# Kernel optimization log

Measured on AMD Instinct MI355X. Metric: run time of the kernel, lower is better.

Reference implementation:

```python
import jax, jax.numpy as jnp
import numpy as np
from jax import lax

S = 8  # num_segments


def conv2d(x, w, stride=1, pad=0):
    return lax.conv_general_dilated(x, w, (stride, stride), [(pad, pad), (pad, pad)],
                                    dimension_numbers=('NCHW', 'OIHW', 'NCHW'))


def bn(x, g, b):  # inference-mode BatchNorm as per-channel affine
    return x * g[None, :, None, None] + b[None, :, None, None]


def conv1x1(x, w):  # w: [O, C]
    return jnp.einsum('bchw,oc->bohw', x, w)


def avgpool3s2(x):  # AvgPool2d(3, stride=2, padding=1), count_include_pad=True
    s = lax.reduce_window(x, 0.0, lax.add, (1, 1, 3, 3), (1, 1, 2, 2),
                          [(0, 0), (0, 0), (1, 1), (1, 1)])
    return s / 9.0


def navigation_mask(x, gumbel, nav_w, nav_bn_g, nav_bn_b, gs_w, gs_b, temp=1.0):
    B = x.shape[0]
    y = x.mean(axis=(2, 3))                                    # global avg pool -> [B, C]
    g = jnp.maximum(y @ nav_w.T * nav_bn_g + nav_bn_b, 0.0)    # conv_pool (1x1) + BN + ReLU -> [B, 2]
    g = g.reshape(B // S, S, 2)
    # grouped 1x1 conv (groups=S) == per-segment 2x2 matmul; gs_w: [S, out, in]
    logits = jnp.einsum('bsi,sji->bsj', g, gs_w) + gs_b        # [nvid, S, 2]
    y_soft = jax.nn.softmax((logits + gumbel) / temp, axis=-1)
    hard = jax.nn.one_hot(jnp.argmax(y_soft, axis=-1), 2, dtype=y_soft.dtype)
    y_st = hard + y_soft - lax.stop_gradient(y_soft)           # straight-through hard gumbel
    return y_st[:, :, 1].reshape(B, 1, 1, 1)                   # channel 1 = focal-on


def setup_inputs() -> dict:
    key = jax.random.key(0)
    ks = iter(jax.random.split(key, 48))

    def rn(shape, scale=0.05):
        return jax.random.normal(next(ks), shape, dtype=jnp.float32) * scale

    B, C_in, C_out, C_amp, H = 128, 64, 128, 64, 56
    u = jax.random.uniform(next(ks), (B // S, S, 2), minval=1e-6, maxval=1.0 - 1e-6)
    return dict(
        x=rn((B, C_in, H, H), 1.0),
        gumbel=(-jnp.log(-jnp.log(u))).astype(jnp.float32),
        nav_w=rn((2, C_in)), nav_bn_g=jnp.ones((2,), jnp.float32), nav_bn_b=jnp.zeros((2,), jnp.float32),
        gs_w=rn((S, 2, 2)),
        gs_b=jnp.tile(jnp.array([1.0, 10.0], dtype=jnp.float32), (S, 1)),  # bias init from source
        ba_w1=rn((C_amp, C_in, 3, 3)), ba_g1=jnp.ones((C_amp,), jnp.float32), ba_b1=jnp.zeros((C_amp,), jnp.float32),
        ba_w2=rn((C_amp, C_amp, 3, 3)), ba_g2=jnp.ones((C_amp,), jnp.float32), ba_b2=jnp.zeros((C_amp,), jnp.float32),
        bf_wd=rn((C_out, C_in)), bf_gd=jnp.ones((C_out,), jnp.float32), bf_bd=jnp.zeros((C_out,), jnp.float32),
        bf_w1=rn((C_out, C_in, 3, 3)), bf_g1=jnp.ones((C_out,), jnp.float32), bf_b1=jnp.zeros((C_out,), jnp.float32),
        bf_w2=rn((C_out, C_out, 3, 3)), bf_g2=jnp.ones((C_out,), jnp.float32), bf_b2=jnp.zeros((C_out,), jnp.float32),
        bt_w=rn((C_out, C_amp)), bt_g=jnp.ones((C_out,), jnp.float32), bt_b=jnp.zeros((C_out,), jnp.float32),
        att_w1=rn((C_out // 16, C_out), 0.01), att_w2=rn((C_out, C_out // 16), 0.01),
        fu_w1=rn((C_out, C_out, 3, 3)), fu_g1=jnp.ones((C_out,), jnp.float32), fu_b1=jnp.zeros((C_out,), jnp.float32),
        fu_w2=rn((C_out, C_out, 3, 3)), fu_g2=jnp.ones((C_out,), jnp.float32), fu_b2=jnp.zeros((C_out,), jnp.float32),
    )


def reference(x, gumbel, nav_w, nav_bn_g, nav_bn_b, gs_w, gs_b,
              ba_w1, ba_g1, ba_b1, ba_w2, ba_g2, ba_b2,
              bf_wd, bf_gd, bf_bd, bf_w1, bf_g1, bf_b1, bf_w2, bf_g2, bf_b2,
              bt_w, bt_g, bt_b, att_w1, att_w2,
              fu_w1, fu_g1, fu_b1, fu_w2, fu_g2, fu_b2):
    mask = navigation_mask(x, gumbel, nav_w, nav_bn_g, nav_bn_b, gs_w, gs_b)
    # ample branch: stride-2 low-res residual block (last_relu=False)
    res_l = avgpool3s2(x)
    h = jnp.maximum(bn(conv2d(x, ba_w1, 2, 1), ba_g1, ba_b1), 0.0)
    x_little = bn(conv2d(h, ba_w2, 1, 1), ba_g2, ba_b2) + res_l              # [B,64,28,28]
    # focal branch: full-res residual block, branch gated per-segment by mask
    res_b = bn(conv1x1(x, bf_wd), bf_gd, bf_bd)
    h = jnp.maximum(bn(conv2d(x, bf_w1, 1, 1), bf_g1, bf_b1), 0.0)
    x_big = res_b + mask * bn(conv2d(h, bf_w2, 1, 1), bf_g2, bf_b2)          # [B,128,56,56]
    x_little = bn(conv1x1(x_little, bt_w), bt_g, bt_b)
    x_little = jnp.repeat(jnp.repeat(x_little, 2, axis=2), 2, axis=3)        # F.interpolate nearest
    # SE-style dynamic fusion
    y = (x_little + x_big).mean(axis=(2, 3))                                 # [B,128]
    att = jax.nn.sigmoid(jnp.maximum(y @ att_w1.T, 0.0) @ att_w2.T)[:, :, None, None]
    out = jnp.maximum(att * x_little + (1.0 - att) * x_big, 0.0)
    # fusion block: residual, last_relu=True
    h = jnp.maximum(bn(conv2d(out, fu_w1, 1, 1), fu_g1, fu_b1), 0.0)
    out = jnp.maximum(bn(conv2d(h, fu_w2, 1, 1), fu_g2, fu_b2) + out, 0.0)
    return out, mask
```

## Files before the change

kernel.cpp:

```cpp
#include <hip/hip_runtime.h>
#include <cstdint>
#include <cstddef>

#define BLK 256

typedef __bf16 bf16x8 __attribute__((ext_vector_type(8)));
typedef float  f32x4  __attribute__((ext_vector_type(4)));

__device__ __forceinline__ float block_reduce_sum(float v, float* sm) {
#pragma unroll
  for (int off = 32; off > 0; off >>= 1) v += __shfl_down(v, off, 64);
  const int lane = threadIdx.x & 63;
  const int wid  = threadIdx.x >> 6;
  if (lane == 0) sm[wid] = v;
  __syncthreads();
  v = sm[0] + sm[1] + sm[2] + sm[3];
  __syncthreads();
  return v;
}

__global__ __launch_bounds__(BLK) void gap_x_k(const float* __restrict__ x,
                                               float* __restrict__ y) {
  __shared__ float sm[4];
  const float4* p4 = reinterpret_cast<const float4*>(x + (size_t)blockIdx.x * 3136);
  float s = 0.f;
  for (int i = threadIdx.x; i < 784; i += BLK) {
    float4 v = p4[i];
    s += (v.x + v.y) + (v.z + v.w);
  }
  s = block_reduce_sum(s, sm);
  if (threadIdx.x == 0) y[blockIdx.x] = s * (1.f / 3136.f);
}

__global__ void mask_k(const float* __restrict__ y, const float* __restrict__ gumbel,
                       const float* __restrict__ nav_w, const float* __restrict__ nbg,
                       const float* __restrict__ nbb, const float* __restrict__ gsw,
                       const float* __restrict__ gsb, float* __restrict__ maskv,
                       float* __restrict__ mask_out) {
  int b = threadIdx.x;
  float d0 = 0.f, d1 = 0.f;
  for (int c = 0; c < 64; ++c) {
    float yv = y[b * 64 + c];
    d0 += yv * nav_w[c];
    d1 += yv * nav_w[64 + c];
  }
  float g0 = fmaxf(d0 * nbg[0] + nbb[0], 0.f);
  float g1 = fmaxf(d1 * nbg[1] + nbb[1], 0.f);
  int vid = b >> 3, s = b & 7;
  float l0 = gsw[s * 4 + 0] * g0 + gsw[s * 4 + 1] * g1 + gsb[s * 2 + 0] + gumbel[(vid * 8 + s) * 2 + 0];
  float l1 = gsw[s * 4 + 2] * g0 + gsw[s * 4 + 3] * g1 + gsb[s * 2 + 1] + gumbel[(vid * 8 + s) * 2 + 1];
  float m = (l1 > l0) ? 1.f : 0.f;
  maskv[b] = m;
  mask_out[b] = m;
}

__global__ __launch_bounds__(BLK) void avgpool_k(const float* __restrict__ x,
                                                 float* __restrict__ out) {
  int idx = blockIdx.x * BLK + threadIdx.x;
  int p = idx % 784;
  int bc = idx / 784;
  int h = p / 28, w = p % 28;
  const float* xp = x + (size_t)bc * 3136;
  int h0 = 2 * h - 1, w0 = 2 * w - 1;
  float s = 0.f;
#pragma unroll
  for (int i = 0; i < 3; ++i) {
    int hh = h0 + i;
    if (hh < 0 || hh >= 56) continue;
#pragma unroll
    for (int j = 0; j < 3; ++j) {
      int ww = w0 + j;
      if (ww < 0 || ww >= 56) continue;
      s += xp[hh * 56 + ww];
    }
  }
  out[idx] = s * (1.f / 9.f);
}

template <int C>
__global__ __launch_bounds__(BLK) void txp_k(const float* __restrict__ src,
                                             __bf16* __restrict__ dst, int NP) {
  __shared__ float t[C * 65];
  const int b = blockIdx.y;
  const int p0 = blockIdx.x * 64;
  for (int i = threadIdx.x; i < C * 64; i += BLK) {
    int c = i >> 6, p = i & 63;
    float v = 0.f;
    if (p0 + p < NP) v = src[((size_t)b * C + c) * NP + p0 + p];
    t[c * 65 + p] = v;
  }
  __syncthreads();
  constexpr int CQ = C / 8;
  for (int i = threadIdx.x; i < 64 * CQ; i += BLK) {
    int cq = i % CQ, pix = i / CQ;
    if (p0 + pix < NP) {
      __bf16 o[8];
#pragma unroll
      for (int j = 0; j < 8; ++j) o[j] = (__bf16)t[(cq * 8 + j) * 65 + pix];
      *reinterpret_cast<uint4*>(dst + ((size_t)b * NP + p0 + pix) * C + cq * 8) =
          *reinterpret_cast<uint4*>(o);
    }
  }
}

__global__ void pack3_k(const float* __restrict__ w, __bf16* __restrict__ dst,
                        int CIN, int MT) {
  int total = (CIN / 32) * 9 * MT * 64;
  int idx = blockIdx.x * BLK + threadIdx.x;
  if (idx >= total) return;
  int lane = idx & 63;
  int g = idx >> 6;
  int mt = g % MT; g /= MT;
  int t = g % 9;  int q = g / 9;
  int oc = mt * 16 + (lane & 15);
  int quad = lane >> 4;
#pragma unroll
  for (int j = 0; j < 8; ++j) {
    int c = q * 32 + quad * 8 + j;
    dst[(size_t)idx * 8 + j] = (__bf16)w[((size_t)oc * CIN + c) * 9 + t];
  }
}

__global__ void pack1_k(const float* __restrict__ w, __bf16* __restrict__ dst,
                        int CIN, int MT) {
  int total = (CIN / 32) * MT * 64;
  int idx = blockIdx.x * BLK + threadIdx.x;
  if (idx >= total) return;
  int lane = idx & 63;
  int g = idx >> 6;
  int mt = g % MT;
  int q = g / MT;
  int oc = mt * 16 + (lane & 15);
  int quad = lane >> 4;
#pragma unroll
  for (int j = 0; j < 8; ++j) {
    int c = q * 32 + quad * 8 + j;
    dst[(size_t)idx * 8 + j] = (__bf16)w[(size_t)oc * CIN + c];
  }
}

template <int W_IMG, int ROWS>
struct Stage {
  static constexpr int COLS  = W_IMG + 2;
  static constexpr int NSLOT = ROWS * COLS * 4;
  static constexpr int NIT   = (NSLOT + BLK - 1) / BLK;
  uint4 R[NIT];

  __device__ __forceinline__ void load(const __bf16* __restrict__ inT, int CIN, int c0,
                                       int img, int h0) {
    constexpr int NPIX = W_IMG * W_IMG;
#pragma unroll
    for (int it = 0; it < NIT; ++it) {
      int s = threadIdx.x + it * BLK;
      uint4 v{0u, 0u, 0u, 0u};
      if (s < NSLOT) {
        int pix = s >> 2, q = s & 3;
        int r = pix / COLS, cc = pix - r * COLS;
        int gh = h0 - 1 + r, gw = cc - 1;
        if (gh >= 0 && gh < W_IMG && gw >= 0 && gw < W_IMG)
          v = *reinterpret_cast<const uint4*>(
              inT + ((size_t)img * NPIX + gh * W_IMG + gw) * CIN + c0 + q * 8);
      }
      R[it] = v;
    }
  }

  __device__ __forceinline__ void store(__bf16* lds) {
#pragma unroll
    for (int it = 0; it < NIT; ++it) {
      int s = threadIdx.x + it * BLK;
      if (s < NSLOT) {
        int pix = s >> 2, q = s & 3;
        *reinterpret_cast<uint4*>(lds + pix * 40 + q * 8) = R[it];
      }
    }
  }
};

template <int W_IMG, int CIN, int MTW, int MODE, int OUTBF, int NSPLIT>
__global__ __launch_bounds__(BLK, 2) void conv3s_bf(
    const __bf16* __restrict__ inT, const __bf16* __restrict__ wp,
    const float* __restrict__ gamma, const float* __restrict__ beta,
    const float* __restrict__ res, void* __restrict__ outv) {
  constexpr int ROWS = 128 / W_IMG + 4;
  constexpr int COLS = W_IMG + 2;
  constexpr int NPIX = W_IMG * W_IMG;
  constexpr int NCH  = CIN / 32;
  constexpr int MT_TOT = MTW * 2;
  constexpr int COUT_B = MT_TOT * 16;
  constexpr int COUT_G = COUT_B * NSPLIT;
  constexpr int MT_TOTG = COUT_G / 16;
  constexpr int NT = (NPIX + 127) / 128;
  constexpr int TILE_E = ROWS * COLS * 40;
  constexpr int LDSE = (OUTBF && 128 * COUT_B > TILE_E) ? 128 * COUT_B : TILE_E;
  __shared__ __bf16 lds[LDSE];

  const int tid = threadIdx.x;
  const int lane = tid & 63, wv = tid >> 6;
  const int wm = wv >> 1, wn = wv & 1;
  const int quad = lane >> 4, li = lane & 15;

  const int F = blockIdx.x + NT * (blockIdx.y + 128 * blockIdx.z);
  constexpr int TOT = NT * 128 * NSPLIT;
  int Wk = (F & 7) * (TOT >> 3) + (F >> 3);
  int bz, u;
  if constexpr (NSPLIT == 2) { bz = Wk & 1; u = Wk >> 1; }
  else                       { bz = 0;      u = Wk;      }
  const int img  = u / NT;
  const int tile = u - img * NT;
  const int P0 = tile * 128;
  const int h0 = P0 / W_IMG;
  const int mtg0 = bz * MT_TOT + wm * MTW;

  int basee[4]; int pstore[4]; bool pok[4];
#pragma unroll
  for (int nt = 0; nt < 4; ++nt) {
    int p = P0 + wn * 64 + nt * 16 + li;
    bool ok = p < NPIX;
    int p2 = ok ? p : (NPIX - 1);
    int h = p2 / W_IMG, w = p2 - h * W_IMG;
    basee[nt] = ((h - h0) * COLS + w) * 40 + quad * 8;
    pstore[nt] = p2; pok[nt] = ok;
  }

  f32x4 acc[MTW][4];
#pragma unroll
  for (int mt = 0; mt < MTW; ++mt)
#pragma unroll
    for (int nt = 0; nt < 4; ++nt) acc[mt][nt] = (f32x4){0.f, 0.f, 0.f, 0.f};

  const bf16x8* wp8 = reinterpret_cast<const bf16x8*>(wp);

  bf16x8 wA[9 * MTW], wB[9 * MTW];
  auto LOADW = [&](bf16x8 (&wr)[9 * MTW], int q) {
#pragma unroll
    for (int t = 0; t < 9; ++t)
#pragma unroll
      for (int mt = 0; mt < MTW; ++mt)
        wr[t * MTW + mt] = wp8[(size_t)((q * 9 + t) * MT_TOTG + mtg0 + mt) * 64 + lane];
  };
  auto TAPS = [&](const bf16x8 (&wr)[9 * MTW]) {
#pragma unroll
    for (int t = 0; t < 9; ++t) {
      const int toff = ((t / 3) * COLS + (t % 3)) * 40;
      bf16x8 xf[4];
#pragma unroll
      for (int nt = 0; nt < 4; ++nt)
        xf[nt] = *reinterpret_cast<const bf16x8*>(&lds[basee[nt] + toff]);
#pragma unroll
      for (int mt = 0; mt < MTW; ++mt)
#pragma unroll
        for (int nt = 0; nt < 4; ++nt)
          acc[mt][nt] = __builtin_amdgcn_mfma_f32_16x16x32_bf16(wr[t * MTW + mt], xf[nt], acc[mt][nt], 0, 0, 0);
    }
  };

  Stage<W_IMG, ROWS> st;
  LOADW(wA, 0);
  __builtin_amdgcn_sched_barrier(0);
  st.load(inT, CIN, 0, img, h0);
  for (int q = 0; q < NCH; q += 2) {
    __syncthreads();
    st.store(lds);
    __syncthreads();
    if (q + 1 < NCH) { st.load(inT, CIN, (q + 1) * 32, img, h0); LOADW(wB, q + 1); }
    TAPS(wA);
    __syncthreads();
    st.store(lds);
    __syncthreads();
    if (q + 2 < NCH) { st.load(inT, CIN, (q + 2) * 32, img, h0); LOADW(wA, q + 2); }
    TAPS(wB);
  }

  if constexpr (!OUTBF) {
    float* out = (float*)outv;
#pragma unroll
    for (int mt = 0; mt < MTW; ++mt) {
#pragma unroll
      for (int r = 0; r < 4; ++r) {
        int oc = bz * COUT_B + wm * MTW * 16 + mt * 16 + quad * 4 + r;
        float g = gamma[oc], bb = beta[oc];
#pragma unroll
        for (int nt = 0; nt < 4; ++nt) {
          if (!pok[nt]) continue;
          size_t idx = ((size_t)img * COUT_G + oc) * NPIX + pstore[nt];
          float v = acc[mt][nt][r] * g + bb;
          if constexpr (MODE == 1 || MODE == 2) v += res[idx];
          if constexpr (MODE == 0 || MODE == 2) v = fmaxf(v, 0.f);
          out[idx] = v;
        }
      }
    }
  } else {
    __bf16* outT = (__bf16*)outv;
    __syncthreads();
#pragma unroll
    for (int mt = 0; mt < MTW; ++mt) {
      int ocl = wm * MTW * 16 + mt * 16 + quad * 4;
      int ocg = bz * COUT_B + ocl;
      float g0 = gamma[ocg + 0], b0 = beta[ocg + 0];
      float g1 = gamma[ocg + 1], b1 = beta[ocg + 1];
      float g2 = gamma[ocg + 2], b2 = beta[ocg + 2];
      float g3 = gamma[ocg + 3], b3 = beta[ocg + 3];
#pragma unroll
      for (int nt = 0; nt < 4; ++nt) {
        if (!pok[nt]) continue;
        int pl = wn * 64 + nt * 16 + li;
        __bf16 o[4];
        o[0] = (__bf16)fmaxf(acc[mt][nt][0] * g0 + b0, 0.f);
        o[1] = (__bf16)fmaxf(acc[mt][nt][1] * g1 + b1, 0.f);
        o[2] = (__bf16)fmaxf(acc[mt][nt][2] * g2 + b2, 0.f);
        o[3] = (__bf16)fmaxf(acc[mt][nt][3] * g3 + b3, 0.f);
        int byt = pl * (COUT_B * 2) + ocl * 2;
        byt ^= (pl & 7) << 4;
        *reinterpret_cast<uint2*>(reinterpret_cast<char*>(lds) + byt) =
            *reinterpret_cast<uint2*>(o);
      }
    }
    __syncthreads();
    constexpr int SLOTS_ROW = COUT_B / 8;
    constexpr int ROWS_PASS = BLK / SLOTS_ROW;
#pragma unroll
    for (int pass = 0; pass < 128 / ROWS_PASS; ++pass) {
      int pl = pass * ROWS_PASS + (tid / SLOTS_ROW);
      int ss = tid % SLOTS_ROW;
      if (P0 + pl < NPIX) {
        int byt = pl * (COUT_B * 2) + ss * 16;
        byt ^= (pl & 7) << 4;
        uint4 vv = *reinterpret_cast<const uint4*>(reinterpret_cast<const char*>(lds) + byt);
        *reinterpret_cast<uint4*>(outT + ((size_t)img * NPIX + P0 + pl) * COUT_G + bz * COUT_B + ss * 8) = vv;
      }
    }
  }
}

__global__ __launch_bounds__(BLK, 2) void conv_ba1_mfma(
    const __bf16* __restrict__ xT, const __bf16* __restrict__ wp,
    const float* __restrict__ gamma, const float* __restrict__ beta,
    __bf16* __restrict__ outT) {
  constexpr int WOUT = 28, NPIX = 784;
  constexpr int ROWS = 13, COLS = 58;
  constexpr int TILE_E = ROWS * COLS * 40;
  __shared__ __bf16 lds[TILE_E];

  const int tid = threadIdx.x;
  const int lane = tid & 63, wv = tid >> 6;
  const int wm = wv >> 1, wn = wv & 1;
  const int quad = lane >> 4, li = lane & 15;
  const int img = blockIdx.y;
  const int P0 = blockIdx.x * 128;
  const int h0 = P0 / WOUT;

  int basee[4]; bool pok[4];
#pragma unroll
  for (int nt = 0; nt < 4; ++nt) {
    int p = P0 + wn * 64 + nt * 16 + li;
    bool ok = p < NPIX;
    int p2 = ok ? p : (NPIX - 1);
    int h = p2 / WOUT, w = p2 - h * WOUT;
    basee[nt] = (2 * (h - h0) * COLS + 2 * w) * 40 + quad * 8;
    pok[nt] = ok;
  }

  f32x4 acc[2][4];
#pragma unroll
  for (int mt = 0; mt < 2; ++mt)
#pragma unroll
    for (int nt = 0; nt < 4; ++nt) acc[mt][nt] = (f32x4){0.f, 0.f, 0.f, 0.f};

  const bf16x8* wp8 = reinterpret_cast<const bf16x8*>(wp);

  bf16x8 wr[18];
  Stage<56, 13> st;
  st.load(xT, 64, 0, img, 2 * h0);
  for (int q = 0; q < 2; ++q) {
    __syncthreads();
    st.store(lds);
    __syncthreads();
#pragma unroll
    for (int t = 0; t < 9; ++t)
#pragma unroll
      for (int mt = 0; mt < 2; ++mt)
        wr[t * 2 + mt] = wp8[(size_t)((q * 9 + t) * 4 + wm * 2 + mt) * 64 + lane];
    __builtin_amdgcn_sched_barrier(0);
    if (q == 0) st.load(xT, 64, 32, img, 2 * h0);
#pragma unroll
    for (int t = 0; t < 9; ++t) {
      const int toff = ((t / 3) * COLS + (t % 3)) * 40;
      bf16x8 xf[4];
#pragma unroll
      for (int nt = 0; nt < 4; ++nt)
        xf[nt] = *reinterpret_cast<const bf16x8*>(&lds[basee[nt] + toff]);
#pragma unroll
      for (int mt = 0; mt < 2; ++mt)
#pragma unroll
        for (int nt = 0; nt < 4; ++nt)
          acc[mt][nt] = __builtin_amdgcn_mfma_f32_16x16x32_bf16(wr[t * 2 + mt], xf[nt], acc[mt][nt], 0, 0, 0);
    }
  }

  __syncthreads();
#pragma unroll
  for (int mt = 0; mt < 2; ++mt) {
    int ocb = wm * 32 + mt * 16 + quad * 4;
    float g0 = gamma[ocb + 0], b0 = beta[ocb + 0];
    float g1 = gamma[ocb + 1], b1 = beta[ocb + 1];
    float g2 = gamma[ocb + 2], b2 = beta[ocb + 2];
    float g3 = gamma[ocb + 3], b3 = beta[ocb + 3];
#pragma unroll
    for (int nt = 0; nt < 4; ++nt) {
      if (!pok[nt]) continue;
      int pl = wn * 64 + nt * 16 + li;
      __bf16 o[4];
      o[0] = (__bf16)fmaxf(acc[mt][nt][0] * g0 + b0, 0.f);
      o[1] = (__bf16)fmaxf(acc[mt][nt][1] * g1 + b1, 0.f);
      o[2] = (__bf16)fmaxf(acc[mt][nt][2] * g2 + b2, 0.f);
      o[3] = (__bf16)fmaxf(acc[mt][nt][3] * g3 + b3, 0.f);
      int byt = pl * 128 + ocb * 2;
      byt ^= (pl & 7) << 4;
      *reinterpret_cast<uint2*>(reinterpret_cast<char*>(lds) + byt) =
          *reinterpret_cast<uint2*>(o);
    }
  }
  __syncthreads();
#pragma unroll
  for (int pass = 0; pass < 4; ++pass) {
    int pl = pass * 32 + (tid >> 3);
    int ss = tid & 7;
    if (P0 + pl < NPIX) {
      int byt = pl * 128 + ss * 16;
      byt ^= (pl & 7) << 4;
      uint4 vv = *reinterpret_cast<const uint4*>(reinterpret_cast<const char*>(lds) + byt);
      *reinterpret_cast<uint4*>(outT + ((size_t)img * NPIX + P0 + pl) * 64 + ss * 8) = vv;
    }
  }
}

__global__ __launch_bounds__(BLK, 2) void conv_xbig_bf(
    const __bf16* __restrict__ hfT, const __bf16* __restrict__ xT,
    const __bf16* __restrict__ wp3, const __bf16* __restrict__ wp1,
    const float* __restrict__ g2v, const float* __restrict__ b2v,
    const float* __restrict__ gdv, const float* __restrict__ bdv,
    const float* __restrict__ maskv, float* __restrict__ out) {
  constexpr int W_IMG = 56, ROWS = 6, COLS = 58, NPIX = 3136, NT = 25;
  __shared__ __bf16 lds[ROWS * COLS * 40];

  const int tid = threadIdx.x;
  const int lane = tid & 63, wv = tid >> 6;
  const int wm = wv >> 1, wn = wv & 1;
  const int quad = lane >> 4, li = lane & 15;

  const int F = blockIdx.x + NT * (blockIdx.y + 128 * blockIdx.z);
  constexpr int TOT = NT * 128 * 2;
  int Wk = (F & 7) * (TOT >> 3) + (F >> 3);
  const int bz = Wk & 1;
  const int u  = Wk >> 1;
  const int img  = u / NT;
  const int tile = u - img * NT;
  const int P0 = tile * 128;
  const int h0 = P0 / W_IMG;
  const float m = maskv[img];

  int basee[4]; int pstore[4]; bool pok[4];
#pragma unroll
  for (int nt = 0; nt < 4; ++nt) {
    int p = P0 + wn * 64 + nt * 16 + li;
    bool ok = p < NPIX;
    int p2 = ok ? p : (NPIX - 1);
    int h = p2 / W_IMG, w = p2 - h * W_IMG;
    basee[nt] = ((h - h0) * COLS + w) * 40 + quad * 8;
    pstore[nt] = p2; pok[nt] = ok;
  }

  f32x4 acc3[2][4], acc1[2][4];
#pragma unroll
  for (int mt = 0; mt < 2; ++mt)
#pragma unroll
    for (int nt = 0; nt < 4; ++nt) {
      acc3[mt][nt] = (f32x4){0.f, 0.f, 0.f, 0.f};
      acc1[mt][nt] = (f32x4){0.f, 0.f, 0.f, 0.f};
    }

  const bf16x8* wp3v = reinterpret_cast<const bf16x8*>(wp3);
  const bf16x8* wp1v = reinterpret_cast<const bf16x8*>(wp1);

  bf16x8 wr[18];
  Stage<56, 6> st;
  st.load(hfT, 128, 0, img, h0);

  for (int q = 0; q < 4; ++q) {
    __syncthreads();
    st.store(lds);
    __syncthreads();
#pragma unroll
    for (int t = 0; t < 9; ++t)
#pragma unroll
      for (int mt = 0; mt < 2; ++mt)
        wr[t * 2 + mt] = wp3v[(size_t)((q * 9 + t) * 8 + bz * 4 + wm * 2 + mt) * 64 + lane];
    __builtin_amdgcn_sched_barrier(0);
    if (q < 3) st.load(hfT, 128, (q + 1) * 32, img, h0);
    else       st.load(xT, 64, 0, img, h0);
#pragma unroll
    for (int t = 0; t < 9; ++t) {
      const int toff = ((t / 3) * COLS + (t % 3)) * 40;
      bf16x8 xf[4];
#pragma unroll
      for (int nt = 0; nt < 4; ++nt)
        xf[nt] = *reinterpret_cast<const bf16x8*>(&lds[basee[nt] + toff]);
#pragma unroll
      for (int mt = 0; mt < 2; ++mt)
#pragma unroll
        for (int nt = 0; nt < 4; ++nt)
          acc3[mt][nt] = __builtin_amdgcn_mfma_f32_16x16x32_bf16(wr[t * 2 + mt], xf[nt], acc3[mt][nt], 0, 0, 0);
    }
  }

  for (int q = 0; q < 2; ++q) {
    __syncthreads();
    st.store(lds);
    __syncthreads();
    bf16x8 w1[2];
#pragma unroll
    for (int mt = 0; mt < 2; ++mt)
      w1[mt] = wp1v[(size_t)(q * 8 + bz * 4 + wm * 2 + mt) * 64 + lane];
    __builtin_amdgcn_sched_barrier(0);
    if (q == 0) st.load(xT, 64, 32, img, h0);
    const int toff = (1 * COLS + 1) * 40;
    bf16x8 xf[4];
#pragma unroll
    for (int nt = 0; nt < 4; ++nt)
      xf[nt] = *reinterpret_cast<const bf16x8*>(&lds[basee[nt] + toff]);
#pragma unroll
    for (int mt = 0; mt < 2; ++mt)
#pragma unroll
      for (int nt = 0; nt < 4; ++nt)
        acc1[mt][nt] = __builtin_amdgcn_mfma_f32_16x16x32_bf16(w1[mt], xf[nt], acc1[mt][nt], 0, 0, 0);
  }

#pragma unroll
  for (int mt = 0; mt < 2; ++mt) {
#pragma unroll
    for (int r = 0; r < 4; ++r) {
      int oc = bz * 64 + wm * 32 + mt * 16 + quad * 4 + r;
      float g2 = g2v[oc], b2 = b2v[oc], gd = gdv[oc], bd = bdv[oc];
#pragma unroll
      for (int nt = 0; nt < 4; ++nt) {
        if (!pok[nt]) continue;
        size_t idx = ((size_t)img * 128 + oc) * NPIX + pstore[nt];
        float v = (acc1[mt][nt][r] * gd + bd) + m * (acc3[mt][nt][r] * g2 + b2);
        out[idx] = v;
      }
    }
  }
}

__global__ __launch_bounds__(BLK) void conv1x1_bt_k(
    const float* __restrict__ xl, const float* __restrict__ w,
    const float* __restrict__ g, const float* __restrict__ bt, float* __restrict__ out) {
  const int b = blockIdx.z;
  const int oc0 = blockIdx.y * 8;
  const float* __restrict__ xp = xl + (size_t)b * 64 * 784;
  float gr[8], br[8];
#pragma unroll
  for (int j = 0; j < 8; ++j) {
    gr[j] = g[oc0 + j];
    br[j] = bt[oc0 + j];
  }
  for (int p = (int)threadIdx.x; p < 784; p += BLK) {
    float acc[8];
#pragma unroll
    for (int j = 0; j < 8; ++j) acc[j] = 0.f;
    for (int c = 0; c < 64; ++c) {
      float xv = xp[c * 784 + p];
#pragma unroll
      for (int j = 0; j < 8; ++j) acc[j] += xv * w[(oc0 + j) * 64 + c];
    }
#pragma unroll
    for (int j = 0; j < 8; ++j)
      out[(size_t)(b * 128 + oc0 + j) * 784 + p] = acc[j] * gr[j] + br[j];
  }
}

__global__ __launch_bounds__(BLK) void gap2_k(const float* __restrict__ xbig,
                                              const float* __restrict__ xlbt,
                                              float* __restrict__ ysum) {
  __shared__ float sm1[4], sm2[4];
  const int bo = blockIdx.x;
  const float4* p4 = reinterpret_cast<const float4*>(xbig + (size_t)bo * 3136);
  float s1 = 0.f;
  for (int i = threadIdx.x; i < 784; i += BLK) {
    float4 v = p4[i];
    s1 += (v.x + v.y) + (v.z + v.w);
  }
  const float4* q4 = reinterpret_cast<const float4*>(xlbt + (size_t)bo * 784);
  float s2 = 0.f;
  for (int i = threadIdx.x; i < 196; i += BLK) {
    float4 v = q4[i];
    s2 += (v.x + v.y) + (v.z + v.w);
  }
  s1 = block_reduce_sum(s1, sm1);
  s2 = block_reduce_sum(s2, sm2);
  if (threadIdx.x == 0) ysum[bo] = s1 * (1.f / 3136.f) + s2 * (1.f / 784.f);
}

__global__ void att_k(const float* __restrict__ ysum, const float* __restrict__ w1,
                      const float* __restrict__ w2, float* __restrict__ att) {
  int b = blockIdx.x;
  int t = threadIdx.x;
  __shared__ float hid[8];
  __shared__ float ybuf[128];
  ybuf[t] = ysum[b * 128 + t];
  __syncthreads();
  if (t < 8) {
    float s = 0.f;
    for (int c = 0; c < 128; ++c) s += ybuf[c] * w1[t * 128 + c];
    hid[t] = fmaxf(s, 0.f);
  }
  __syncthreads();
  float s = 0.f;
#pragma unroll
  for (int j = 0; j < 8; ++j) s += hid[j] * w2[t * 8 + j];
  att[b * 128 + t] = 1.f / (1.f + expf(-s));
}

__global__ __launch_bounds__(BLK) void se_k(const float* __restrict__ xlbt,
                                            const float* __restrict__ att,
                                            float* __restrict__ out) {
  int idx = blockIdx.x * BLK + threadIdx.x;
  int p = idx % 3136;
  int bo = idx / 3136;
  int h = p / 56, w = p % 56;
  float a = att[bo];
  float xl = xlbt[(size_t)bo * 784 + (h >> 1) * 28 + (w >> 1)];
  float xb = out[idx];
  out[idx] = fmaxf(a * xl + (1.f - a) * xb, 0.f);
}

extern "C" void kernel_launch(void* const* d_in, const int* in_sizes, int n_in,
                              void* d_out, int out_size, void* d_ws, size_t ws_size,
                              hipStream_t stream) {
  const float* x      = (const float*)d_in[0];
  const float* gumbel = (const float*)d_in[1];
  const float* nav_w  = (const float*)d_in[2];
  const float* nbg    = (const float*)d_in[3];
  const float* nbb    = (const float*)d_in[4];
  const float* gsw    = (const float*)d_in[5];
  const float* gsb    = (const float*)d_in[6];
  const float* ba_w1  = (const float*)d_in[7];
  const float* ba_g1  = (const float*)d_in[8];
  const float* ba_b1  = (const float*)d_in[9];
  const float* ba_w2  = (const float*)d_in[10];
  const float* ba_g2  = (const float*)d_in[11];
  const float* ba_b2  = (const float*)d_in[12];
  const float* bf_wd  = (const float*)d_in[13];
  const float* bf_gd  = (const float*)d_in[14];
  const float* bf_bd  = (const float*)d_in[15];
  const float* bf_w1  = (const float*)d_in[16];
  const float* bf_g1  = (const float*)d_in[17];
  const float* bf_b1  = (const float*)d_in[18];
  const float* bf_w2  = (const float*)d_in[19];
  const float* bf_g2  = (const float*)d_in[20];
  const float* bf_b2  = (const float*)d_in[21];
  const float* bt_w   = (const float*)d_in[22];
  const float* bt_g   = (const float*)d_in[23];
  const float* bt_b   = (const float*)d_in[24];
  const float* att_w1 = (const float*)d_in[25];
  const float* att_w2 = (const float*)d_in[26];
  const float* fu_w1  = (const float*)d_in[27];
  const float* fu_g1  = (const float*)d_in[28];
  const float* fu_b1  = (const float*)d_in[29];
  const float* fu_w2  = (const float*)d_in[30];
  const float* fu_g2  = (const float*)d_in[31];
  const float* fu_b2  = (const float*)d_in[32];

  float* out = (float*)d_out;
  float* ws  = (float*)d_ws;

  const size_t N_OUT = 51380224;
  float* bufA = ws;
  __bf16* hfbf  = (__bf16*)bufA;
  __bf16* hfubf = (__bf16*)bufA;
  __bf16* xbf   = (__bf16*)(bufA + 25690112);
  __bf16* outbf = (__bf16*)(bufA + 25690112);
  float* xlbt = bufA + N_OUT;
  float* resl = xlbt + 12845056;
  __bf16* habf = (__bf16*)(resl + 6422528);
  float* ygap = resl + 6422528 + 6422528;
  float* mskv = ygap + 8192;
  float* ysum = mskv + 128;
  float* attb = ysum + 16384;
  float* wend = attb + 16384;
  __bf16* wsW1 = (__bf16*)(wend);
  __bf16* wsW2 = (__bf16*)(wend + 36864);
  __bf16* wsF1 = (__bf16*)(wend + 110592);
  __bf16* wsF2 = (__bf16*)(wend + 184320);
  __bf16* wsA2 = (__bf16*)(wend + 258048);
  __bf16* wsWd = (__bf16*)(wend + 276480);
  __bf16* wsA1 = (__bf16*)(wend + 280576);
  float* mask_out = out + ((size_t)out_size - 128);

  pack3_k<<<36, BLK, 0, stream>>>(bf_w1, wsW1, 64, 8);
  pack3_k<<<72, BLK, 0, stream>>>(bf_w2, wsW2, 128, 8);
  pack3_k<<<72, BLK, 0, stream>>>(fu_w1, wsF1, 128, 8);
  pack3_k<<<72, BLK, 0, stream>>>(fu_w2, wsF2, 128, 8);
  pack3_k<<<18, BLK, 0, stream>>>(ba_w2, wsA2, 64, 4);
  pack3_k<<<18, BLK, 0, stream>>>(ba_w1, wsA1, 64, 4);
  pack1_k<<<4, BLK, 0, stream>>>(bf_wd, wsWd, 64, 8);

  txp_k<64><<<dim3(49, 128), BLK, 0, stream>>>(x, xbf, 3136);

  gap_x_k<<<8192, BLK, 0, stream>>>(x, ygap);
  mask_k<<<1, 128, 0, stream>>>(ygap, gumbel, nav_w, nbg, nbb, gsw, gsb, mskv, mask_out);

  avgpool_k<<<25088, BLK, 0, stream>>>(x, resl);
  conv_ba1_mfma<<<dim3(7, 128), BLK, 0, stream>>>(xbf, wsA1, ba_g1, ba_b1, habf);
  conv3s_bf<28, 64, 2, 1, 0, 1><<<dim3(7, 128), BLK, 0, stream>>>(
      habf, wsA2, ba_g2, ba_b2, resl, resl);
  conv1x1_bt_k<<<dim3(1, 16, 128), BLK, 0, stream>>>(resl, bt_w, bt_g, bt_b, xlbt);

  conv3s_bf<56, 64, 2, 0, 1, 2><<<dim3(25, 128, 2), BLK, 0, stream>>>(
      xbf, wsW1, bf_g1, bf_b1, nullptr, hfbf);
  conv_xbig_bf<<<dim3(25, 128, 2), BLK, 0, stream>>>(
      hfbf, xbf, wsW2, wsWd, bf_g2, bf_b2, bf_gd, bf_bd, mskv, out);

  gap2_k<<<16384, BLK, 0, stream>>>(out, xlbt, ysum);
  att_k<<<128, 128, 0, stream>>>(ysum, att_w1, att_w2, attb);
  se_k<<<200704, BLK, 0, stream>>>(xlbt, attb, out);

  txp_k<128><<<dim3(49, 128), BLK, 0, stream>>>(out, outbf, 3136);

  conv3s_bf<56, 128, 2, 0, 1, 2><<<dim3(25, 128, 2), BLK, 0, stream>>>(
      outbf, wsF1, fu_g1, fu_b1, nullptr, hfubf);
  conv3s_bf<56, 128, 2, 2, 0, 2><<<dim3(25, 128, 2), BLK, 0, stream>>>(
      hfubf, wsF2, fu_g2, fu_b2, out, out);
}
```

Measured before the change: 1.860 ms.

## Fuse SE gating into transpose and cut conv weight double-buffering for occupancy

The SE-fusion elementwise pass is merged into the fp32-to-bf16 NHWC transpose kernel, so the fused output is read once and both the fp32 result and the bf16 copy are written from one pass. The conv3s_bf main loop drops its double-buffered weight registers and loads weights once per channel chunk. Launch bounds for conv3s_bf and conv_xbig_bf are raised to three blocks per SM. Together these aim for higher occupancy, at the cost of exposing weight-load latency inside each iteration.

```diff
diff --git a/kernel.cpp b/kernel.cpp
--- a/kernel.cpp
+++ b/kernel.cpp
@@ -100,6 +100,36 @@
       *reinterpret_cast<uint4*>(dst + ((size_t)b * NP + p0 + pix) * C + cq * 8) =
           *reinterpret_cast<uint4*>(o);
     }
+  }
+}
+
+__global__ __launch_bounds__(BLK) void txpse_k(float* __restrict__ outio,
+                                               const float* __restrict__ xlbt,
+                                               const float* __restrict__ att,
+                                               __bf16* __restrict__ dst) {
+  __shared__ float t[128 * 65];
+  const int b = blockIdx.y;
+  const int p0 = blockIdx.x * 64;
+  for (int i = threadIdx.x; i < 128 * 64; i += BLK) {
+    int c = i >> 6, p = i & 63;
+    int pg = p0 + p;
+    size_t idx = ((size_t)b * 128 + c) * 3136 + pg;
+    float v = outio[idx];
+    int h = pg / 56, w = pg - h * 56;
+    float xl = xlbt[((size_t)b * 128 + c) * 784 + (h >> 1) * 28 + (w >> 1)];
+    float a = att[b * 128 + c];
+    float r = fmaxf(a * xl + (1.f - a) * v, 0.f);
+    outio[idx] = r;
+    t[c * 65 + p] = r;
+  }
+  __syncthreads();
+  for (int i = threadIdx.x; i < 64 * 16; i += BLK) {
+    int cq = i % 16, pix = i / 16;
+    __bf16 o[8];
+#pragma unroll
+    for (int j = 0; j < 8; ++j) o[j] = (__bf16)t[(cq * 8 + j) * 65 + pix];
+    *reinterpret_cast<uint4*>(dst + ((size_t)b * 3136 + p0 + pix) * 128 + cq * 8) =
+        *reinterpret_cast<uint4*>(o);
   }
 }
 
@@ -178,7 +208,7 @@
 };
 
 template <int W_IMG, int CIN, int MTW, int MODE, int OUTBF, int NSPLIT>
-__global__ __launch_bounds__(BLK, 2) void conv3s_bf(
+__global__ __launch_bounds__(BLK, 3) void conv3s_bf(
     const __bf16* __restrict__ inT, const __bf16* __restrict__ wp,
     const float* __restrict__ gamma, const float* __restrict__ beta,
     const float* __restrict__ res, void* __restrict__ outv) {
@@ -231,15 +261,20 @@
 
   const bf16x8* wp8 = reinterpret_cast<const bf16x8*>(wp);
 
-  bf16x8 wA[9 * MTW], wB[9 * MTW];
-  auto LOADW = [&](bf16x8 (&wr)[9 * MTW], int q) {
+  bf16x8 wr[9 * MTW];
+  Stage<W_IMG, ROWS> st;
+  st.load(inT, CIN, 0, img, h0);
+  for (int q = 0; q < NCH; ++q) {
+    __syncthreads();
+    st.store(lds);
+    __syncthreads();
 #pragma unroll
     for (int t = 0; t < 9; ++t)
 #pragma unroll
       for (int mt = 0; mt < MTW; ++mt)
         wr[t * MTW + mt] = wp8[(size_t)((q * 9 + t) * MT_TOTG + mtg0 + mt) * 64 + lane];
-  };
-  auto TAPS = [&](const bf16x8 (&wr)[9 * MTW]) {
+    __builtin_amdgcn_sched_barrier(0);
+    if (q + 1 < NCH) st.load(inT, CIN, (q + 1) * 32, img, h0);
 #pragma unroll
     for (int t = 0; t < 9; ++t) {
       const int toff = ((t / 3) * COLS + (t % 3)) * 40;
@@ -253,23 +288,6 @@
         for (int nt = 0; nt < 4; ++nt)
           acc[mt][nt] = __builtin_amdgcn_mfma_f32_16x16x32_bf16(wr[t * MTW + mt], xf[nt], acc[mt][nt], 0, 0, 0);
     }
-  };
-
-  Stage<W_IMG, ROWS> st;
-  LOADW(wA, 0);
-  __builtin_amdgcn_sched_barrier(0);
-  st.load(inT, CIN, 0, img, h0);
-  for (int q = 0; q < NCH; q += 2) {
-    __syncthreads();
-    st.store(lds);
-    __syncthreads();
-    if (q + 1 < NCH) { st.load(inT, CIN, (q + 1) * 32, img, h0); LOADW(wB, q + 1); }
-    TAPS(wA);
-    __syncthreads();
-    st.store(lds);
-    __syncthreads();
-    if (q + 2 < NCH) { st.load(inT, CIN, (q + 2) * 32, img, h0); LOADW(wA, q + 2); }
-    TAPS(wB);
   }
 
   if constexpr (!OUTBF) {
@@ -436,7 +454,7 @@
   }
 }
 
-__global__ __launch_bounds__(BLK, 2) void conv_xbig_bf(
+__global__ __launch_bounds__(BLK, 3) void conv_xbig_bf(
     const __bf16* __restrict__ hfT, const __bf16* __restrict__ xT,
     const __bf16* __restrict__ wp3, const __bf16* __restrict__ wp1,
     const float* __restrict__ g2v, const float* __restrict__ b2v,
@@ -621,19 +639,6 @@
 #pragma unroll
   for (int j = 0; j < 8; ++j) s += hid[j] * w2[t * 8 + j];
   att[b * 128 + t] = 1.f / (1.f + expf(-s));
-}
-
-__global__ __launch_bounds__(BLK) void se_k(const float* __restrict__ xlbt,
-                                            const float* __restrict__ att,
-                                            float* __restrict__ out) {
-  int idx = blockIdx.x * BLK + threadIdx.x;
-  int p = idx % 3136;
-  int bo = idx / 3136;
-  int h = p / 56, w = p % 56;
-  float a = att[bo];
-  float xl = xlbt[(size_t)bo * 784 + (h >> 1) * 28 + (w >> 1)];
-  float xb = out[idx];
-  out[idx] = fmaxf(a * xl + (1.f - a) * xb, 0.f);
 }
 
 extern "C" void kernel_launch(void* const* d_in, const int* in_sizes, int n_in,
@@ -725,9 +730,7 @@
 
   gap2_k<<<16384, BLK, 0, stream>>>(out, xlbt, ysum);
   att_k<<<128, 128, 0, stream>>>(ysum, att_w1, att_w2, attb);
-  se_k<<<200704, BLK, 0, stream>>>(xlbt, attb, out);
-
-  txp_k<128><<<dim3(49, 128), BLK, 0, stream>>>(out, outbf, 3136);
+  txpse_k<<<dim3(49, 128), BLK, 0, stream>>>(out, xlbt, attb, outbf);
 
   conv3s_bf<56, 128, 2, 0, 1, 2><<<dim3(25, 128, 2), BLK, 0, stream>>>(
       outbf, wsF1, fu_g1, fu_b1, nullptr, hfubf);
```

Measured after the change: 1.795 ms. 3.5% less time.
